# Kernel optimization log

Measured on AMD Instinct MI355X. Metric: run time of the kernel, lower is better.

The kernel has to match this reference:

```python
import jax, jax.numpy as jnp
import numpy as np

B, N, C, HEADS, WS = 8, 16384, 256, 8, 8


def setup_inputs() -> dict:
    key = jax.random.key(0)
    ks = jax.random.split(key, 8)
    s = 0.02
    eye = jnp.eye(HEADS, dtype=jnp.float32)
    return {
        "x": jax.random.normal(ks[0], (B, N, C), jnp.float32),
        "query": jax.random.normal(ks[1], (B, N, C), jnp.float32),
        "W_qk": jax.random.normal(ks[2], (2 * C, C), jnp.float32) * s,
        "W_v": jax.random.normal(ks[3], (C, C), jnp.float32) * s,
        "W_proj": jax.random.normal(ks[4], (C, C), jnp.float32) * s,
        "b_proj": jnp.zeros((C,), jnp.float32),
        "W_pre": eye + jax.random.normal(ks[5], (HEADS, HEADS), jnp.float32) * s,
        "W_post": eye + jax.random.normal(ks[6], (HEADS, HEADS), jnp.float32) * s,
        "H": 128,
        "W": 128,
    }


def reference(x, query, W_qk, W_v, W_proj, b_proj, W_pre, W_post, H, W):
    B_, N_, C_ = x.shape
    h, ws = HEADS, WS
    d = C_ // h
    hg, wg = H // ws, W // ws
    G, S = hg * wg, ws * ws  # windows, tokens per window

    def window(t):
        # [B,N,C] -> [B,G,S,C] with S = ws*ws window tokens
        t = t.reshape(B_, hg, ws, wg, ws, C_).transpose(0, 1, 3, 2, 4, 5)
        return t.reshape(B_, G, S, C_)

    xw, qw = window(x), window(query)
    qk = qw @ W_qk.T                                   # [B,G,S,2C]
    q = qk[..., :C_].reshape(B_, G, S, h, d)
    k = qk[..., C_:].reshape(B_, G, S, h, d)
    v = (xw @ W_v.T).reshape(B_, G, S, h, d)

    scale = d ** -0.5
    attn = jnp.einsum('bgqhd,bgkhd->bgqkh', q, k) * scale  # heads last
    attn = attn @ W_pre.T                               # pre-softmax talking heads
    attn = jax.nn.softmax(attn, axis=-2)                # softmax over key dim
    attn = attn @ W_post.T                              # post-softmax talking heads

    out = jnp.einsum('bgqkh,bgkhd->bgqhd', attn, v).reshape(B_, G, S, C_)
    # un-window: [B,G,S,C] -> [B,N,C]
    out = out.reshape(B_, hg, wg, ws, ws, C_).transpose(0, 1, 3, 2, 4, 5)
    out = out.reshape(B_, N_, C_)
    return out @ W_proj.T + b_proj
```

## Files before the change

### kernel.cpp

```cpp
#include <hip/hip_runtime.h>

using u16 = unsigned short;
using u32 = unsigned int;

typedef __bf16 bf16x8 __attribute__((ext_vector_type(8)));
typedef float  f32x4  __attribute__((ext_vector_type(4)));
typedef u16    u16x4  __attribute__((ext_vector_type(4)));
typedef u16    u16x8  __attribute__((ext_vector_type(8)));

#define MFMA16(a,b,c) __builtin_amdgcn_mfma_f32_16x16x32_bf16((a),(b),(c),0,0,0)

__device__ __forceinline__ u16 f2bf(float f){
    u32 u = __builtin_bit_cast(u32,f);
    u += 0x7FFFu + ((u>>16)&1u);
    return (u16)(u>>16);
}

#define QKSCALE 0.17677669529663687f

#define SA    264
#define VTS   72
#define SC_QS 556
#define SC_HS 68
#define P_QS  520

#define OFF_RA   0
#define OFF_RB   36864
#define OFF_ATT  (36864 + 16*P_QS*2)
#define OFF_WPRE  70656
#define OFF_WPOST 70912
#define OFF_BP    71168
#define OFF_INV   72192
#define LDS_BYTES 72704

#define WS_WQK 0
#define WS_WV  131072
#define WS_WPJ 196608
#define WS_ELEMS 262144

__global__ __launch_bounds__(256) void convert_weights(
    const float* __restrict__ wqk, const float* __restrict__ wv,
    const float* __restrict__ wproj, u16* __restrict__ ws)
{
    for (int i = blockIdx.x*256 + threadIdx.x; i < WS_ELEMS; i += gridDim.x*256){
        float v;
        if (i < 131072){
            v = wqk[i];
            if (i < 65536) v *= QKSCALE;
        } else if (i < 196608) v = wv[i - 131072];
        else                   v = wproj[i - 196608];
        ws[i] = f2bf(v);
    }
}

template<bool WF32>
__device__ __forceinline__ bf16x8 ldb(const void* w, size_t off){
    if constexpr (!WF32) return *(const bf16x8*)((const u16*)w + off);
    const float* p = (const float*)w + off;
    f32x4 a = *(const f32x4*)p;
    f32x4 b = *(const f32x4*)(p + 4);
    u16x8 r;
    r[0]=f2bf(a[0]); r[1]=f2bf(a[1]); r[2]=f2bf(a[2]); r[3]=f2bf(a[3]);
    r[4]=f2bf(b[0]); r[5]=f2bf(b[1]); r[6]=f2bf(b[2]); r[7]=f2bf(b[3]);
    return __builtin_bit_cast(bf16x8, r);
}

template<bool WF32>
__global__ __launch_bounds__(512, 4) void gta_kernel(
    const float* __restrict__ x, const float* __restrict__ query,
    const void* __restrict__ wqk, const void* __restrict__ wv,
    const void* __restrict__ wproj, const float* __restrict__ bproj,
    const float* __restrict__ wpre, const float* __restrict__ wpost,
    float* __restrict__ outp)
{
    extern __shared__ char smem[];
    u16*   sRA  = (u16*)(smem + OFF_RA);
    float* sSc  = (float*)(smem + OFF_RA);
    u16*   sRB  = (u16*)(smem + OFF_RB);
    u16*   sP   = (u16*)(smem + OFF_RB);
    u16*   sAtt = (u16*)(smem + OFF_ATT);
    float* sWpre  = (float*)(smem + OFF_WPRE);
    float* sWpost = (float*)(smem + OFF_WPOST);
    float* sBp    = (float*)(smem + OFF_BP);
    float* sInv   = (float*)(smem + OFF_INV);

    const int tid  = threadIdx.x;
    const int wid  = tid >> 6;
    const int lane = tid & 63;
    const int quad = lane >> 4;
    const int l16  = lane & 15;
    const int h    = wid;

    const int bid = blockIdx.x;
    const int b  = bid >> 8;
    const int g  = bid & 255;
    const int gr = g >> 4, gc = g & 15;

    const int stok = tid >> 3, sseg = tid & 7;
    const int srow = gr*8 + (stok>>3), scol = gc*8 + (stok&7);
    const size_t sgbase = (((size_t)b*16384) + (size_t)(srow*128 + scol))*256 + sseg*32;

    {
        const float* gx = x + sgbase;
        #pragma unroll
        for (int i=0;i<4;i++){
            f32x4 a = *(const f32x4*)(gx + i*8);
            f32x4 c = *(const f32x4*)(gx + i*8 + 4);
            u16x8 v;
            v[0]=f2bf(a[0]); v[1]=f2bf(a[1]); v[2]=f2bf(a[2]); v[3]=f2bf(a[3]);
            v[4]=f2bf(c[0]); v[5]=f2bf(c[1]); v[6]=f2bf(c[2]); v[7]=f2bf(c[3]);
            *(u16x8*)(sRB + stok*SA + sseg*32 + i*8) = v;
        }
    }
    if (tid < 64)       sWpre[tid]     = wpre[tid];
    else if (tid < 128) sWpost[tid-64] = wpost[tid-64];
    if (tid < 256)      sBp[tid]       = bproj[tid];
    __syncthreads();

    #pragma unroll 1
    for (int i=0;i<2;i++){
        const int ct = wid + 8*i;
        const size_t wbase = (size_t)(ct*16 + l16)*256 + quad*8;
        f32x4 acc0={0.f,0.f,0.f,0.f}, acc1=acc0, acc2=acc0, acc3=acc0;
        #pragma unroll
        for (int ks=0; ks<8; ks++){
            bf16x8 bc = ldb<WF32>(wv, wbase + (size_t)ks*32);
            const int ko = ks*32 + quad*8;
            bf16x8 a0 = *(const bf16x8*)(sRB + ( 0+l16)*SA + ko);
            bf16x8 a1 = *(const bf16x8*)(sRB + (16+l16)*SA + ko);
            bf16x8 a2 = *(const bf16x8*)(sRB + (32+l16)*SA + ko);
            bf16x8 a3 = *(const bf16x8*)(sRB + (48+l16)*SA + ko);
            acc0 = MFMA16(a0, bc, acc0);
            acc1 = MFMA16(a1, bc, acc1);
            acc2 = MFMA16(a2, bc, acc2);
            acc3 = MFMA16(a3, bc, acc3);
        }
        const int c = ct*16 + l16;
        #pragma unroll
        for (int rt=0; rt<4; rt++){
            f32x4 a = (rt==0)?acc0:(rt==1)?acc1:(rt==2)?acc2:acc3;
            u16x4 pk; pk[0]=f2bf(a[0]); pk[1]=f2bf(a[1]); pk[2]=f2bf(a[2]); pk[3]=f2bf(a[3]);
            *(u16x4*)(sRA + c*VTS + rt*16 + quad*4) = pk;
        }
    }
    __syncthreads();

    bf16x8 Vh[2][2];
    #pragma unroll
    for (int ks=0; ks<2; ks++)
        #pragma unroll
        for (int ct=0; ct<2; ct++)
            Vh[ks][ct] = *(const bf16x8*)(sRA + (h*32 + ct*16 + l16)*VTS + ks*32 + quad*8);
    {
        const float* gq = query + sgbase;
        #pragma unroll
        for (int i=0;i<4;i++){
            f32x4 a = *(const f32x4*)(gq + i*8);
            f32x4 c = *(const f32x4*)(gq + i*8 + 4);
            u16x8 v;
            v[0]=f2bf(a[0]); v[1]=f2bf(a[1]); v[2]=f2bf(a[2]); v[3]=f2bf(a[3]);
            v[4]=f2bf(c[0]); v[5]=f2bf(c[1]); v[6]=f2bf(c[2]); v[7]=f2bf(c[3]);
            *(u16x8*)(sRB + stok*SA + sseg*32 + i*8) = v;
        }
    }
    __syncthreads();

    #pragma unroll 1
    for (int i=0;i<2;i++){
        const int ct = wid + 8*i;
        const size_t wbase = (size_t)(ct*16 + l16)*256 + quad*8;
        f32x4 acc0={0.f,0.f,0.f,0.f}, acc1=acc0, acc2=acc0, acc3=acc0;
        #pragma unroll
        for (int ks=0; ks<8; ks++){
            bf16x8 bc = ldb<WF32>(wqk, wbase + (size_t)ks*32);
            const int ko = ks*32 + quad*8;
            bf16x8 a0 = *(const bf16x8*)(sRB + ( 0+l16)*SA + ko);
            bf16x8 a1 = *(const bf16x8*)(sRB + (16+l16)*SA + ko);
            bf16x8 a2 = *(const bf16x8*)(sRB + (32+l16)*SA + ko);
            bf16x8 a3 = *(const bf16x8*)(sRB + (48+l16)*SA + ko);
            acc0 = MFMA16(a0, bc, acc0);
            acc1 = MFMA16(a1, bc, acc1);
            acc2 = MFMA16(a2, bc, acc2);
            acc3 = MFMA16(a3, bc, acc3);
        }
        const int cc = ct*16 + l16;
        #pragma unroll
        for (int rt=0; rt<4; rt++){
            f32x4 a = (rt==0)?acc0:(rt==1)?acc1:(rt==2)?acc2:acc3;
            #pragma unroll
            for (int r=0;r<4;r++)
                sRA[(rt*16 + quad*4 + r)*SA + cc] = f2bf(a[r]);
        }
    }
    __syncthreads();

    bf16x8 Qh[4];
    #pragma unroll
    for (int p=0; p<4; p++)
        Qh[p] = *(const bf16x8*)(sRA + (p*16 + l16)*SA + h*32 + quad*8);
    __syncthreads();

    #pragma unroll 1
    for (int i=0;i<2;i++){
        const int ct = wid + 8*i;
        const size_t wbase = (size_t)(256 + ct*16 + l16)*256 + quad*8;
        f32x4 acc0={0.f,0.f,0.f,0.f}, acc1=acc0, acc2=acc0, acc3=acc0;
        #pragma unroll
        for (int ks=0; ks<8; ks++){
            bf16x8 bc = ldb<WF32>(wqk, wbase + (size_t)ks*32);
            const int ko = ks*32 + quad*8;
            bf16x8 a0 = *(const bf16x8*)(sRB + ( 0+l16)*SA + ko);
            bf16x8 a1 = *(const bf16x8*)(sRB + (16+l16)*SA + ko);
            bf16x8 a2 = *(const bf16x8*)(sRB + (32+l16)*SA + ko);
            bf16x8 a3 = *(const bf16x8*)(sRB + (48+l16)*SA + ko);
            acc0 = MFMA16(a0, bc, acc0);
            acc1 = MFMA16(a1, bc, acc1);
            acc2 = MFMA16(a2, bc, acc2);
            acc3 = MFMA16(a3, bc, acc3);
        }
        const int cc = ct*16 + l16;
        #pragma unroll
        for (int rt=0; rt<4; rt++){
            f32x4 a = (rt==0)?acc0:(rt==1)?acc1:(rt==2)?acc2:acc3;
            #pragma unroll
            for (int r=0;r<4;r++)
                sRA[(rt*16 + quad*4 + r)*SA + cc] = f2bf(a[r]);
        }
    }
    __syncthreads();

    bf16x8 Kh[4];
    #pragma unroll
    for (int kt=0; kt<4; kt++)
        Kh[kt] = *(const bf16x8*)(sRA + (kt*16 + l16)*SA + h*32 + quad*8);
    __syncthreads();

    #pragma unroll 1
    for (int p=0; p<4; p++){
        #pragma unroll
        for (int kt=0; kt<4; kt++){
            f32x4 z = {0.f,0.f,0.f,0.f};
            f32x4 d = MFMA16(Qh[p], Kh[kt], z);
            #pragma unroll
            for (int r=0;r<4;r++)
                sSc[(quad*4 + r)*SC_QS + h*SC_HS + kt*16 + l16] = d[r];
        }
        __syncthreads();
        #pragma unroll
        for (int i=0;i<2;i++){
            const int pp = tid + i*512;
            const int q = pp >> 6, k = pp & 63;
            float* rowp = sSc + q*SC_QS + k;
            float s0[8];
            #pragma unroll
            for (int hh=0;hh<8;hh++){
                float v = rowp[hh*SC_HS];
                if constexpr (WF32) v *= QKSCALE;
                s0[hh] = v;
            }
            #pragma unroll
            for (int hp=0;hp<8;hp++){
                float m = 0.f;
                #pragma unroll
                for (int hh=0;hh<8;hh++) m += sWpre[hp*8+hh]*s0[hh];
                rowp[hp*SC_HS] = m;
            }
        }
        __syncthreads();
        if (tid < 256){
            const int q = tid>>4, hh = (tid>>1)&7, half = tid&1;
            f32x4* r4 = (f32x4*)(sSc + q*SC_QS + hh*SC_HS + half*32);
            float mx = -1e30f;
            #pragma unroll
            for (int i=0;i<8;i++){ f32x4 v=r4[i];
                mx = fmaxf(mx, fmaxf(fmaxf(v[0],v[1]), fmaxf(v[2],v[3]))); }
            mx = fmaxf(mx, __shfl_xor(mx, 1));
            float sum = 0.f;
            #pragma unroll
            for (int i=0;i<8;i++){ f32x4 v=r4[i]; f32x4 e;
                e[0]=__expf(v[0]-mx); e[1]=__expf(v[1]-mx);
                e[2]=__expf(v[2]-mx); e[3]=__expf(v[3]-mx);
                sum += e[0]+e[1]+e[2]+e[3]; r4[i]=e; }
            sum += __shfl_xor(sum, 1);
            if (!half) sInv[q*8 + hh] = 1.f/sum;
        }
        __syncthreads();
        #pragma unroll
        for (int i=0;i<2;i++){
            const int pp = tid + i*512;
            const int q = pp >> 6, k = pp & 63;
            const float* rowp = sSc + q*SC_QS + k;
            float s0[8];
            #pragma unroll
            for (int hh=0;hh<8;hh++) s0[hh] = rowp[hh*SC_HS] * sInv[q*8+hh];
            #pragma unroll
            for (int hp=0;hp<8;hp++){
                float m = 0.f;
                #pragma unroll
                for (int hh=0;hh<8;hh++) m += sWpost[hp*8+hh]*s0[hh];
                sP[q*P_QS + hp*64 + k] = f2bf(m);
            }
        }
        __syncthreads();
        #pragma unroll
        for (int ct=0; ct<2; ct++){
            f32x4 acc = {0.f,0.f,0.f,0.f};
            #pragma unroll
            for (int ks=0; ks<2; ks++){
                bf16x8 ap = *(const bf16x8*)(sP + l16*P_QS + h*64 + ks*32 + quad*8);
                acc = MFMA16(ap, Vh[ks][ct], acc);
            }
            #pragma unroll
            for (int r=0;r<4;r++)
                sAtt[(quad*4 + r)*SA + h*32 + ct*16 + l16] = f2bf(acc[r]);
        }
        __syncthreads();
        #pragma unroll
        for (int i=0;i<2;i++){
            const int ct2 = wid + 8*i;
            const size_t wbase = (size_t)(ct2*16 + l16)*256 + quad*8;
            f32x4 acc = {0.f,0.f,0.f,0.f};
            #pragma unroll
            for (int ks=0; ks<8; ks++){
                bf16x8 a = *(const bf16x8*)(sAtt + l16*SA + ks*32 + quad*8);
                bf16x8 bc = ldb<WF32>(wproj, wbase + (size_t)ks*32);
                acc = MFMA16(a, bc, acc);
            }
            const int n = ct2*16 + l16;
            const float bias = sBp[n];
            #pragma unroll
            for (int r=0;r<4;r++){
                const int wtok = p*16 + quad*4 + r;
                const int rrow = gr*8 + (wtok>>3), ccol = gc*8 + (wtok&7);
                outp[(((size_t)b*16384) + (size_t)(rrow*128 + ccol))*256 + n] = acc[r] + bias;
            }
        }
    }
}

extern "C" void kernel_launch(void* const* d_in, const int* in_sizes, int n_in,
                              void* d_out, int out_size, void* d_ws, size_t ws_size,
                              hipStream_t stream) {
    (void)in_sizes; (void)n_in; (void)out_size;
    const float* x     = (const float*)d_in[0];
    const float* query = (const float*)d_in[1];
    const float* wqk   = (const float*)d_in[2];
    const float* wv    = (const float*)d_in[3];
    const float* wproj = (const float*)d_in[4];
    const float* bproj = (const float*)d_in[5];
    const float* wpre  = (const float*)d_in[6];
    const float* wpost = (const float*)d_in[7];
    float* outp = (float*)d_out;

    if (ws_size >= (size_t)WS_ELEMS*2){
        u16* ws = (u16*)d_ws;
        convert_weights<<<256, 256, 0, stream>>>(wqk, wv, wproj, ws);
        hipFuncSetAttribute((const void*)gta_kernel<false>,
                            hipFuncAttributeMaxDynamicSharedMemorySize, LDS_BYTES);
        gta_kernel<false><<<2048, 512, LDS_BYTES, stream>>>(
            x, query, ws + WS_WQK, ws + WS_WV, ws + WS_WPJ,
            bproj, wpre, wpost, outp);
    } else {
        hipFuncSetAttribute((const void*)gta_kernel<true>,
                            hipFuncAttributeMaxDynamicSharedMemorySize, LDS_BYTES);
        gta_kernel<true><<<2048, 512, LDS_BYTES, stream>>>(
            x, query, wqk, wv, wproj, bproj, wpre, wpost, outp);
    }
}
```

Baseline: 629.7 us.

## Compute per-head Q/K/V in registers, prefetch query, stage coalesced output stores

Each warp now computes only its own head's V, Q and K projection columns directly, converting MFMA outputs into operand layout through a small per-warp LDS scratch. This removes the full-window LDS round trips and several block barriers, and the smaller LDS footprint may allow more resident blocks. The query tile is prefetched into registers while the V projection runs. Output projection results are staged in LDS so global stores become 32-byte contiguous vector writes instead of scattered scalar writes. The cost is higher register pressure from the extra accumulators and the prefetched query.

```diff
diff --git a/kernel.cpp b/kernel.cpp
--- a/kernel.cpp
+++ b/kernel.cpp
@@ -16,22 +16,26 @@
     return (u16)(u>>16);
 }
 
+__device__ __forceinline__ u16x4 pack4(f32x4 a){
+    u16x4 p; p[0]=f2bf(a[0]); p[1]=f2bf(a[1]); p[2]=f2bf(a[2]); p[3]=f2bf(a[3]);
+    return p;
+}
+
 #define QKSCALE 0.17677669529663687f
 
 #define SA    264
-#define VTS   72
-#define SC_QS 556
+#define SC_QS 548
 #define SC_HS 68
 #define P_QS  520
-
-#define OFF_RA   0
-#define OFF_RB   36864
-#define OFF_ATT  (36864 + 16*P_QS*2)
-#define OFF_WPRE  70656
-#define OFF_WPOST 70912
-#define OFF_BP    71168
-#define OFF_INV   72192
-#define LDS_BYTES 72704
+#define OP_S  260
+#define SCR_W 40
+
+#define R2_OFF    35072
+#define OFF_WPRE  51712
+#define OFF_WPOST 51968
+#define OFF_BP    52224
+#define OFF_INV   53248
+#define LDS_BYTES 53760
 
 #define WS_WQK 0
 #define WS_WV  131072
@@ -74,11 +78,11 @@
     float* __restrict__ outp)
 {
     extern __shared__ char smem[];
-    u16*   sRA  = (u16*)(smem + OFF_RA);
-    float* sSc  = (float*)(smem + OFF_RA);
-    u16*   sRB  = (u16*)(smem + OFF_RB);
-    u16*   sP   = (u16*)(smem + OFF_RB);
-    u16*   sAtt = (u16*)(smem + OFF_ATT);
+    u16*   sStage = (u16*)(smem);
+    float* sSc    = (float*)(smem);
+    u16*   sAtt   = (u16*)(smem);
+    u16*   sP     = (u16*)(smem + R2_OFF);
+    float* sOp    = (float*)(smem + R2_OFF);
     float* sWpre  = (float*)(smem + OFF_WPRE);
     float* sWpost = (float*)(smem + OFF_WPOST);
     float* sBp    = (float*)(smem + OFF_BP);
@@ -100,6 +104,8 @@
     const int srow = gr*8 + (stok>>3), scol = gc*8 + (stok&7);
     const size_t sgbase = (((size_t)b*16384) + (size_t)(srow*128 + scol))*256 + sseg*32;
 
+    u16* scr = (u16*)(smem + R2_OFF) + wid*(16*SCR_W);
+
     {
         const float* gx = x + sgbase;
         #pragma unroll
@@ -109,7 +115,7 @@
             u16x8 v;
             v[0]=f2bf(a[0]); v[1]=f2bf(a[1]); v[2]=f2bf(a[2]); v[3]=f2bf(a[3]);
             v[4]=f2bf(c[0]); v[5]=f2bf(c[1]); v[6]=f2bf(c[2]); v[7]=f2bf(c[3]);
-            *(u16x8*)(sRB + stok*SA + sseg*32 + i*8) = v;
+            *(u16x8*)(sStage + stok*SA + sseg*32 + i*8) = v;
         }
     }
     if (tid < 64)       sWpre[tid]     = wpre[tid];
@@ -117,122 +123,99 @@
     if (tid < 256)      sBp[tid]       = bproj[tid];
     __syncthreads();
 
-    #pragma unroll 1
-    for (int i=0;i<2;i++){
-        const int ct = wid + 8*i;
-        const size_t wbase = (size_t)(ct*16 + l16)*256 + quad*8;
-        f32x4 acc0={0.f,0.f,0.f,0.f}, acc1=acc0, acc2=acc0, acc3=acc0;
+    const float bias0 = sBp[wid*16 + l16];
+    const float bias1 = sBp[(wid+8)*16 + l16];
+
+    f32x4 qreg[8];
+    {
+        const float* gq = query + sgbase;
+        #pragma unroll
+        for (int i=0;i<4;i++){
+            qreg[2*i]   = *(const f32x4*)(gq + i*8);
+            qreg[2*i+1] = *(const f32x4*)(gq + i*8 + 4);
+        }
+    }
+
+    bf16x8 Vh[2][2];
+    {
+        f32x4 va[2][4];
+        #pragma unroll
+        for (int c=0;c<2;c++)
+            #pragma unroll
+            for (int rt=0;rt<4;rt++) va[c][rt] = (f32x4){0.f,0.f,0.f,0.f};
         #pragma unroll
         for (int ks=0; ks<8; ks++){
-            bf16x8 bc = ldb<WF32>(wv, wbase + (size_t)ks*32);
+            bf16x8 w0 = ldb<WF32>(wv, (size_t)(h*32      + l16)*256 + ks*32 + quad*8);
+            bf16x8 w1 = ldb<WF32>(wv, (size_t)(h*32 + 16 + l16)*256 + ks*32 + quad*8);
             const int ko = ks*32 + quad*8;
-            bf16x8 a0 = *(const bf16x8*)(sRB + ( 0+l16)*SA + ko);
-            bf16x8 a1 = *(const bf16x8*)(sRB + (16+l16)*SA + ko);
-            bf16x8 a2 = *(const bf16x8*)(sRB + (32+l16)*SA + ko);
-            bf16x8 a3 = *(const bf16x8*)(sRB + (48+l16)*SA + ko);
-            acc0 = MFMA16(a0, bc, acc0);
-            acc1 = MFMA16(a1, bc, acc1);
-            acc2 = MFMA16(a2, bc, acc2);
-            acc3 = MFMA16(a3, bc, acc3);
-        }
-        const int c = ct*16 + l16;
-        #pragma unroll
-        for (int rt=0; rt<4; rt++){
-            f32x4 a = (rt==0)?acc0:(rt==1)?acc1:(rt==2)?acc2:acc3;
-            u16x4 pk; pk[0]=f2bf(a[0]); pk[1]=f2bf(a[1]); pk[2]=f2bf(a[2]); pk[3]=f2bf(a[3]);
-            *(u16x4*)(sRA + c*VTS + rt*16 + quad*4) = pk;
+            #pragma unroll
+            for (int rt=0; rt<4; rt++){
+                bf16x8 a = *(const bf16x8*)(sStage + (rt*16+l16)*SA + ko);
+                va[0][rt] = MFMA16(a, w0, va[0][rt]);
+                va[1][rt] = MFMA16(a, w1, va[1][rt]);
+            }
+        }
+        #pragma unroll
+        for (int ctl=0; ctl<2; ctl++){
+            #pragma unroll
+            for (int ksh=0; ksh<2; ksh++){
+                *(u16x4*)(scr + l16*SCR_W +      quad*4) = pack4(va[ctl][ksh*2  ]);
+                *(u16x4*)(scr + l16*SCR_W + 16 + quad*4) = pack4(va[ctl][ksh*2+1]);
+                Vh[ksh][ctl] = *(const bf16x8*)(scr + l16*SCR_W + quad*8);
+            }
         }
     }
     __syncthreads();
 
-    bf16x8 Vh[2][2];
-    #pragma unroll
-    for (int ks=0; ks<2; ks++)
-        #pragma unroll
-        for (int ct=0; ct<2; ct++)
-            Vh[ks][ct] = *(const bf16x8*)(sRA + (h*32 + ct*16 + l16)*VTS + ks*32 + quad*8);
-    {
-        const float* gq = query + sgbase;
+    {
         #pragma unroll
         for (int i=0;i<4;i++){
-            f32x4 a = *(const f32x4*)(gq + i*8);
-            f32x4 c = *(const f32x4*)(gq + i*8 + 4);
+            f32x4 a = qreg[2*i], c = qreg[2*i+1];
             u16x8 v;
             v[0]=f2bf(a[0]); v[1]=f2bf(a[1]); v[2]=f2bf(a[2]); v[3]=f2bf(a[3]);
             v[4]=f2bf(c[0]); v[5]=f2bf(c[1]); v[6]=f2bf(c[2]); v[7]=f2bf(c[3]);
-            *(u16x8*)(sRB + stok*SA + sseg*32 + i*8) = v;
+            *(u16x8*)(sStage + stok*SA + sseg*32 + i*8) = v;
         }
     }
     __syncthreads();
 
-    #pragma unroll 1
-    for (int i=0;i<2;i++){
-        const int ct = wid + 8*i;
-        const size_t wbase = (size_t)(ct*16 + l16)*256 + quad*8;
-        f32x4 acc0={0.f,0.f,0.f,0.f}, acc1=acc0, acc2=acc0, acc3=acc0;
+    bf16x8 Qh[4], Kh[4];
+    {
+        f32x4 qa[2][4], ka[2][4];
+        #pragma unroll
+        for (int c=0;c<2;c++)
+            #pragma unroll
+            for (int t=0;t<4;t++){ qa[c][t] = (f32x4){0.f,0.f,0.f,0.f}; ka[c][t] = qa[c][t]; }
         #pragma unroll
         for (int ks=0; ks<8; ks++){
-            bf16x8 bc = ldb<WF32>(wqk, wbase + (size_t)ks*32);
+            const size_t ro = (size_t)(h*32 + l16)*256 + ks*32 + quad*8;
+            bf16x8 wq0 = ldb<WF32>(wqk, ro);
+            bf16x8 wq1 = ldb<WF32>(wqk, ro + 16*256);
+            bf16x8 wk0 = ldb<WF32>(wqk, ro + 65536);
+            bf16x8 wk1 = ldb<WF32>(wqk, ro + 65536 + 16*256);
             const int ko = ks*32 + quad*8;
-            bf16x8 a0 = *(const bf16x8*)(sRB + ( 0+l16)*SA + ko);
-            bf16x8 a1 = *(const bf16x8*)(sRB + (16+l16)*SA + ko);
-            bf16x8 a2 = *(const bf16x8*)(sRB + (32+l16)*SA + ko);
-            bf16x8 a3 = *(const bf16x8*)(sRB + (48+l16)*SA + ko);
-            acc0 = MFMA16(a0, bc, acc0);
-            acc1 = MFMA16(a1, bc, acc1);
-            acc2 = MFMA16(a2, bc, acc2);
-            acc3 = MFMA16(a3, bc, acc3);
-        }
-        const int cc = ct*16 + l16;
-        #pragma unroll
-        for (int rt=0; rt<4; rt++){
-            f32x4 a = (rt==0)?acc0:(rt==1)?acc1:(rt==2)?acc2:acc3;
-            #pragma unroll
-            for (int r=0;r<4;r++)
-                sRA[(rt*16 + quad*4 + r)*SA + cc] = f2bf(a[r]);
-        }
-    }
-    __syncthreads();
-
-    bf16x8 Qh[4];
-    #pragma unroll
-    for (int p=0; p<4; p++)
-        Qh[p] = *(const bf16x8*)(sRA + (p*16 + l16)*SA + h*32 + quad*8);
-    __syncthreads();
-
-    #pragma unroll 1
-    for (int i=0;i<2;i++){
-        const int ct = wid + 8*i;
-        const size_t wbase = (size_t)(256 + ct*16 + l16)*256 + quad*8;
-        f32x4 acc0={0.f,0.f,0.f,0.f}, acc1=acc0, acc2=acc0, acc3=acc0;
-        #pragma unroll
-        for (int ks=0; ks<8; ks++){
-            bf16x8 bc = ldb<WF32>(wqk, wbase + (size_t)ks*32);
-            const int ko = ks*32 + quad*8;
-            bf16x8 a0 = *(const bf16x8*)(sRB + ( 0+l16)*SA + ko);
-            bf16x8 a1 = *(const bf16x8*)(sRB + (16+l16)*SA + ko);
-            bf16x8 a2 = *(const bf16x8*)(sRB + (32+l16)*SA + ko);
-            bf16x8 a3 = *(const bf16x8*)(sRB + (48+l16)*SA + ko);
-            acc0 = MFMA16(a0, bc, acc0);
-            acc1 = MFMA16(a1, bc, acc1);
-            acc2 = MFMA16(a2, bc, acc2);
-            acc3 = MFMA16(a3, bc, acc3);
-        }
-        const int cc = ct*16 + l16;
-        #pragma unroll
-        for (int rt=0; rt<4; rt++){
-            f32x4 a = (rt==0)?acc0:(rt==1)?acc1:(rt==2)?acc2:acc3;
-            #pragma unroll
-            for (int r=0;r<4;r++)
-                sRA[(rt*16 + quad*4 + r)*SA + cc] = f2bf(a[r]);
-        }
-    }
-    __syncthreads();
-
-    bf16x8 Kh[4];
-    #pragma unroll
-    for (int kt=0; kt<4; kt++)
-        Kh[kt] = *(const bf16x8*)(sRA + (kt*16 + l16)*SA + h*32 + quad*8);
+            #pragma unroll
+            for (int t=0; t<4; t++){
+                bf16x8 bx = *(const bf16x8*)(sStage + (t*16+l16)*SA + ko);
+                qa[0][t] = MFMA16(wq0, bx, qa[0][t]);
+                qa[1][t] = MFMA16(wq1, bx, qa[1][t]);
+                ka[0][t] = MFMA16(wk0, bx, ka[0][t]);
+                ka[1][t] = MFMA16(wk1, bx, ka[1][t]);
+            }
+        }
+        #pragma unroll
+        for (int t=0; t<4; t++){
+            *(u16x4*)(scr + l16*SCR_W +      quad*4) = pack4(qa[0][t]);
+            *(u16x4*)(scr + l16*SCR_W + 16 + quad*4) = pack4(qa[1][t]);
+            Qh[t] = *(const bf16x8*)(scr + l16*SCR_W + quad*8);
+        }
+        #pragma unroll
+        for (int t=0; t<4; t++){
+            *(u16x4*)(scr + l16*SCR_W +      quad*4) = pack4(ka[0][t]);
+            *(u16x4*)(scr + l16*SCR_W + 16 + quad*4) = pack4(ka[1][t]);
+            Kh[t] = *(const bf16x8*)(scr + l16*SCR_W + quad*8);
+        }
+    }
     __syncthreads();
 
     #pragma unroll 1
@@ -315,25 +298,32 @@
                 sAtt[(quad*4 + r)*SA + h*32 + ct*16 + l16] = f2bf(acc[r]);
         }
         __syncthreads();
-        #pragma unroll
-        for (int i=0;i<2;i++){
-            const int ct2 = wid + 8*i;
-            const size_t wbase = (size_t)(ct2*16 + l16)*256 + quad*8;
-            f32x4 acc = {0.f,0.f,0.f,0.f};
+        {
+            f32x4 o0 = {0.f,0.f,0.f,0.f}, o1 = o0;
             #pragma unroll
             for (int ks=0; ks<8; ks++){
-                bf16x8 a = *(const bf16x8*)(sAtt + l16*SA + ks*32 + quad*8);
-                bf16x8 bc = ldb<WF32>(wproj, wbase + (size_t)ks*32);
-                acc = MFMA16(a, bc, acc);
-            }
-            const int n = ct2*16 + l16;
-            const float bias = sBp[n];
+                bf16x8 a  = *(const bf16x8*)(sAtt + l16*SA + ks*32 + quad*8);
+                bf16x8 w0 = ldb<WF32>(wproj, (size_t)((wid  )*16 + l16)*256 + ks*32 + quad*8);
+                bf16x8 w1 = ldb<WF32>(wproj, (size_t)((wid+8)*16 + l16)*256 + ks*32 + quad*8);
+                o0 = MFMA16(a, w0, o0);
+                o1 = MFMA16(a, w1, o1);
+            }
             #pragma unroll
             for (int r=0;r<4;r++){
-                const int wtok = p*16 + quad*4 + r;
-                const int rrow = gr*8 + (wtok>>3), ccol = gc*8 + (wtok&7);
-                outp[(((size_t)b*16384) + (size_t)(rrow*128 + ccol))*256 + n] = acc[r] + bias;
-            }
+                sOp[(quad*4+r)*OP_S + wid*16 + l16]     = o0[r] + bias0;
+                sOp[(quad*4+r)*OP_S + (wid+8)*16 + l16] = o1[r] + bias1;
+            }
+        }
+        __syncthreads();
+        {
+            const int wtok = p*16 + (tid>>5);
+            const int useg = tid & 31;
+            const int rrow = gr*8 + (wtok>>3), ccol = gc*8 + (wtok&7);
+            float* dst = outp + (((size_t)b*16384) + (size_t)(rrow*128 + ccol))*256 + useg*8;
+            f32x4 v0 = *(const f32x4*)(sOp + (tid>>5)*OP_S + useg*8);
+            f32x4 v1 = *(const f32x4*)(sOp + (tid>>5)*OP_S + useg*8 + 4);
+            *(f32x4*)(dst)     = v0;
+            *(f32x4*)(dst + 4) = v1;
         }
     }
 }
```

Result: no change. 636.3 us (+1.0%).
